# Optimization experiments

Measured on AMD Instinct MI355X. Metric: run time of the kernel, lower is better.

## Reference

```python
import jax, jax.numpy as jnp
import numpy as np

H = 2048; FF = 8192; NH = 16; HD = 128; R = 16; SCALING = 2.0  # alpha/r = 32/16
EPS = 1e-5
NLEV = 15.0  # 2**4 - 1 levels for 4-bit quantization

def _quantize(key, out_f, in_f):
    # mirrors QuantizedLinear.quantize_weights on a randn*0.02 init weight
    w = jax.random.normal(key, (out_f, in_f), dtype=jnp.float32) * 0.02
    wmin = w.min(axis=1, keepdims=True)
    wmax = w.max(axis=1, keepdims=True)
    rng = jnp.clip(wmax - wmin, 1e-6)
    sc = rng / NLEV
    q = jnp.clip(jnp.round((w - wmin) / sc), 0, NLEV).astype(jnp.int8)
    return q, sc[:, 0], wmin[:, 0]

def setup_inputs():
    key = jax.random.key(0)
    ks = jax.random.split(key, 22)
    dims = [('q', H, H), ('k', H, H), ('v', H, H), ('o', H, H), ('g', FF, H), ('u', FF, H), ('d', H, FF)]
    d = {}
    i = 0
    for name, of, inf in dims:
        qw, sc, zp = _quantize(ks[i], of, inf); i += 1
        d[name + '_qw'] = qw; d[name + '_sc'] = sc; d[name + '_zp'] = zp
        d[name + '_A'] = jax.random.normal(ks[i], (R, inf), dtype=jnp.float32) * 0.01; i += 1
        d[name + '_B'] = jax.random.normal(ks[i], (of, R), dtype=jnp.float32) * 0.01; i += 1
    d['x'] = jax.random.normal(ks[i], (2, 2048, H), dtype=jnp.float32)
    d['ln1_w'] = jnp.ones(H); d['ln1_b'] = jnp.zeros(H)
    d['ln2_w'] = jnp.ones(H); d['ln2_b'] = jnp.zeros(H)
    return d

def _forward(x, qws, ps, lns):
    def lin(h, i):
        sc, zp, A, B = ps[i]
        # dequantize int8 weight (per-row scale/zero-point) + LoRA low-rank update
        W = qws[i].astype(jnp.float32) * sc[:, None] + zp[:, None] + (B @ A) * SCALING
        return h @ W.T
    def ln(h, w, b):
        mu = h.mean(-1, keepdims=True)
        var = h.var(-1, keepdims=True)  # biased, matches torch LayerNorm
        return (h - mu) / jnp.sqrt(var + EPS) * w + b
    ln1_w, ln1_b, ln2_w, ln2_b = lns
    Bsz, S, _ = x.shape
    h = ln(x, ln1_w, ln1_b)
    q = lin(h, 0).reshape(Bsz, S, NH, HD)
    k = lin(h, 1).reshape(Bsz, S, NH, HD)
    v = lin(h, 2).reshape(Bsz, S, NH, HD)
    attn = jnp.einsum('bqhd,bkhd->bhqk', q, k) / (HD ** 0.5)
    attn = jax.nn.softmax(attn, axis=-1)  # dropout is identity in eval
    o = jnp.einsum('bhqk,bkhd->bqhd', attn, v).reshape(Bsz, S, H)
    x1 = x + lin(o, 3)
    h2 = ln(x1, ln2_w, ln2_b)
    ff = jax.nn.silu(lin(h2, 4)) * lin(h2, 5)
    return x1 + lin(ff, 6)

def reference(x, q_qw, q_sc, q_zp, q_A, q_B, k_qw, k_sc, k_zp, k_A, k_B, v_qw, v_sc, v_zp, v_A, v_B, o_qw, o_sc, o_zp, o_A, o_B, g_qw, g_sc, g_zp, g_A, g_B, u_qw, u_sc, u_zp, u_A, u_B, d_qw, d_sc, d_zp, d_A, d_B, ln1_w, ln1_b, ln2_w, ln2_b):
    qws = (q_qw, k_qw, v_qw, o_qw, g_qw, u_qw, d_qw)
    ps = [(q_sc, q_zp, q_A, q_B), (k_sc, k_zp, k_A, k_B), (v_sc, v_zp, v_A, v_B), (o_sc, o_zp, o_A, o_B), (g_sc, g_zp, g_A, g_B), (u_sc, u_zp, u_A, u_B), (d_sc, d_zp, d_A, d_B)]
    return _forward(x, qws, ps, (ln1_w, ln1_b, ln2_w, ln2_b))
```

## Files before the change

### kernel.cpp

```cpp
#include <hip/hip_runtime.h>
#include <cstdint>
#include <cstddef>

#define GLOBAL_AS __attribute__((address_space(1)))
#define LDS_AS    __attribute__((address_space(3)))

typedef __bf16 bf16;
typedef __bf16 bf16x4 __attribute__((ext_vector_type(4)));
typedef __bf16 bf16x8 __attribute__((ext_vector_type(8)));
typedef float  f32x4  __attribute__((ext_vector_type(4)));
typedef int    i32x4  __attribute__((ext_vector_type(4)));
typedef unsigned int u32x2 __attribute__((ext_vector_type(2)));

__device__ __forceinline__ void gl_lds16(const void* g, void* l) {
  __builtin_amdgcn_global_load_lds((GLOBAL_AS void*)g, (LDS_AS void*)l, 16, 0, 0);
}

__global__ __launch_bounds__(256) void ln_kernel(const float* __restrict__ x,
                                                 const float* __restrict__ w,
                                                 const float* __restrict__ bias,
                                                 bf16* __restrict__ out) {
  const int row = blockIdx.x;
  const int tid = threadIdx.x;
  const float* xr = x + (size_t)row * 2048;
  f32x4 v0 = ((const f32x4*)xr)[tid * 2];
  f32x4 v1 = ((const f32x4*)xr)[tid * 2 + 1];
  float s = 0.f, ss = 0.f;
#pragma unroll
  for (int j = 0; j < 4; ++j) { s += v0[j]; ss += v0[j] * v0[j]; }
#pragma unroll
  for (int j = 0; j < 4; ++j) { s += v1[j]; ss += v1[j] * v1[j]; }
#pragma unroll
  for (int d = 1; d < 64; d <<= 1) { s += __shfl_xor(s, d); ss += __shfl_xor(ss, d); }
  __shared__ float red[8];
  const int wave = tid >> 6, lane = tid & 63;
  if (lane == 0) { red[wave * 2] = s; red[wave * 2 + 1] = ss; }
  __syncthreads();
  s  = red[0] + red[2] + red[4] + red[6];
  ss = red[1] + red[3] + red[5] + red[7];
  const float mean = s * (1.f / 2048.f);
  const float var  = ss * (1.f / 2048.f) - mean * mean;
  const float rstd = rsqrtf(var + 1e-5f);
  const int col = tid * 8;
  bf16x8 o;
#pragma unroll
  for (int j = 0; j < 4; ++j) o[j]     = (bf16)((v0[j] - mean) * rstd * w[col + j]     + bias[col + j]);
#pragma unroll
  for (int j = 0; j < 4; ++j) o[4 + j] = (bf16)((v1[j] - mean) * rstd * w[col + 4 + j] + bias[col + 4 + j]);
  *(bf16x8*)(out + (size_t)row * 2048 + col) = o;
}

__global__ __launch_bounds__(256) void ln_q_kernel(const float* __restrict__ x,
    const float* __restrict__ w, const float* __restrict__ bias,
    char* __restrict__ qh, float* __restrict__ s_m, float* __restrict__ rs,
    float* __restrict__ de) {
  const int row = blockIdx.x;
  const int tid = threadIdx.x;
  const float* xr = x + (size_t)row * 2048;
  f32x4 v0 = ((const f32x4*)xr)[tid * 2];
  f32x4 v1 = ((const f32x4*)xr)[tid * 2 + 1];
  float s = 0.f, ss = 0.f;
#pragma unroll
  for (int j = 0; j < 4; ++j) { s += v0[j]; ss += v0[j] * v0[j]; }
#pragma unroll
  for (int j = 0; j < 4; ++j) { s += v1[j]; ss += v1[j] * v1[j]; }
#pragma unroll
  for (int d = 1; d < 64; d <<= 1) { s += __shfl_xor(s, d); ss += __shfl_xor(ss, d); }
  __shared__ float red[12];
  const int wave = tid >> 6, lane = tid & 63;
  if (lane == 0) { red[wave * 2] = s; red[wave * 2 + 1] = ss; }
  __syncthreads();
  s  = red[0] + red[2] + red[4] + red[6];
  ss = red[1] + red[3] + red[5] + red[7];
  const float mean = s * (1.f / 2048.f);
  const float var  = ss * (1.f / 2048.f) - mean * mean;
  const float rstd = rsqrtf(var + 1e-5f);
  const int col = tid * 8;
  float y[8];
#pragma unroll
  for (int j = 0; j < 4; ++j) y[j]     = (v0[j] - mean) * rstd * w[col + j]     + bias[col + j];
#pragma unroll
  for (int j = 0; j < 4; ++j) y[4 + j] = (v1[j] - mean) * rstd * w[col + 4 + j] + bias[col + 4 + j];
  float sy = 0.f, mx = 0.f;
#pragma unroll
  for (int j = 0; j < 8; ++j) { sy += y[j]; mx = fmaxf(mx, fabsf(y[j])); }
#pragma unroll
  for (int d = 1; d < 64; d <<= 1) { sy += __shfl_xor(sy, d); mx = fmaxf(mx, __shfl_xor(mx, d)); }
  __syncthreads();
  if (lane == 0) { red[wave * 2] = sy; red[wave * 2 + 1] = mx; }
  __syncthreads();
  const float sya = red[0] + red[2] + red[4] + red[6];
  const float mxa = fmaxf(fmaxf(red[1], red[3]), fmaxf(red[5], red[7]));
  const float inv = 127.f / fmaxf(mxa, 1e-8f);
  unsigned int lo = 0, hi = 0;
  int qs = 0;
#pragma unroll
  for (int j = 0; j < 4; ++j) { int qi = (int)rintf(y[j] * inv);     qs += qi; lo |= ((unsigned int)qi & 0xffu) << (8 * j); }
#pragma unroll
  for (int j = 0; j < 4; ++j) { int qi = (int)rintf(y[4 + j] * inv); qs += qi; hi |= ((unsigned int)qi & 0xffu) << (8 * j); }
  u32x2 st; st[0] = lo; st[1] = hi;
  *(u32x2*)(qh + (size_t)row * 2048 + col) = st;
  float fqs = (float)qs;
#pragma unroll
  for (int d = 1; d < 64; d <<= 1) fqs += __shfl_xor(fqs, d);
  __syncthreads();
  if (lane == 0) red[8 + wave] = fqs;
  __syncthreads();
  if (tid == 0) {
    const float qsa = red[8] + red[9] + red[10] + red[11];
    const float smv = fmaxf(mxa, 1e-8f) / 127.f;
    s_m[row] = smv; rs[row] = sya; de[row] = sya - smv * qsa;
  }
}

__global__ __launch_bounds__(256) void dequant_kernel(const int* __restrict__ qw,
    const float* __restrict__ sc, const float* __restrict__ zp,
    const float* __restrict__ A, const float* __restrict__ Bm,
    bf16* __restrict__ W, int out_f, int in_f) {
  const int per_row = in_f >> 3;
  const int idx = blockIdx.x * 256 + threadIdx.x;
  const int o  = idx / per_row;
  const int i0 = (idx - o * per_row) << 3;
  const float s = sc[o], z = zp[o];
  float bl[16];
#pragma unroll
  for (int r = 0; r < 16; ++r) bl[r] = Bm[o * 16 + r];
  float acc[8] = {0.f, 0.f, 0.f, 0.f, 0.f, 0.f, 0.f, 0.f};
#pragma unroll
  for (int r = 0; r < 16; ++r) {
    const f32x4* ap = (const f32x4*)(A + (size_t)r * in_f + i0);
    f32x4 a0 = ap[0], a1 = ap[1];
#pragma unroll
    for (int j = 0; j < 4; ++j) { acc[j] += bl[r] * a0[j]; acc[4 + j] += bl[r] * a1[j]; }
  }
  const int* qp = qw + (size_t)o * in_f + i0;
  bf16x8 w8;
#pragma unroll
  for (int j = 0; j < 8; ++j) w8[j] = (bf16)((float)qp[j] * s + z + 2.f * acc[j]);
  *(bf16x8*)(W + (size_t)o * in_f + i0) = w8;
}

__global__ __launch_bounds__(256) void pack_w_kernel(const int* __restrict__ qw,
    const float* __restrict__ sc, char* __restrict__ out, float* __restrict__ wsum) {
  const int row = blockIdx.x;
  const int tid = threadIdx.x;
  const size_t idx = (size_t)row * 2048 + tid * 8;
  i32x4 a = *(const i32x4*)(qw + idx);
  i32x4 b = *(const i32x4*)(qw + idx + 4);
  unsigned int lo = ((unsigned)a[0] & 0xffu) | (((unsigned)a[1] & 0xffu) << 8) |
                    (((unsigned)a[2] & 0xffu) << 16) | (((unsigned)a[3] & 0xffu) << 24);
  unsigned int hi = ((unsigned)b[0] & 0xffu) | (((unsigned)b[1] & 0xffu) << 8) |
                    (((unsigned)b[2] & 0xffu) << 16) | (((unsigned)b[3] & 0xffu) << 24);
  u32x2 st; st[0] = lo; st[1] = hi;
  *(u32x2*)(out + idx) = st;
  float fs = (float)(a[0] + a[1] + a[2] + a[3] + b[0] + b[1] + b[2] + b[3]);
#pragma unroll
  for (int d = 1; d < 64; d <<= 1) fs += __shfl_xor(fs, d);
  __shared__ float red[4];
  const int wave = tid >> 6, lane = tid & 63;
  if (lane == 0) red[wave] = fs;
  __syncthreads();
  if (tid == 0) wsum[row] = sc[row] * (red[0] + red[1] + red[2] + red[3]) * (1.f / 2048.f);
}

__global__ __launch_bounds__(256) void pack_b2_kernel(const float* __restrict__ gB,
    const float* __restrict__ uB, bf16* __restrict__ B2g, bf16* __restrict__ B2u) {
  const int idx = blockIdx.x * 256 + threadIdx.x;
  const int nn = idx >> 5, r = idx & 31;
  B2g[idx] = (r < 16)  ? (bf16)(2.f * gB[nn * 16 + r])        : (bf16)0.f;
  B2u[idx] = (r >= 16) ? (bf16)(2.f * uB[nn * 16 + (r - 16)]) : (bf16)0.f;
}

__global__ __launch_bounds__(256) void hA_kernel(const char* __restrict__ qh,
    const float* __restrict__ s_m, const float* __restrict__ Ag,
    const float* __restrict__ Au, bf16* __restrict__ hA) {
  __shared__ bf16 Asm[32 * 512];
  const int tid = threadIdx.x, wave = tid >> 6, lane = tid & 63;
  const int row = blockIdx.x * 4 + wave;
  float acc[32];
#pragma unroll
  for (int r = 0; r < 32; ++r) acc[r] = 0.f;
  for (int kb = 0; kb < 2048; kb += 512) {
    const int r2 = tid >> 3, c0 = (tid & 7) * 64;
    const float* src = (r2 < 16 ? Ag + (size_t)r2 * 2048 : Au + (size_t)(r2 - 16) * 2048) + kb + c0;
#pragma unroll
    for (int j = 0; j < 64; j += 8) {
      f32x4 va = *(const f32x4*)(src + j);
      f32x4 vb = *(const f32x4*)(src + j + 4);
      bf16x8 bv;
#pragma unroll
      for (int jj = 0; jj < 4; ++jj) { bv[jj] = (bf16)va[jj]; bv[4 + jj] = (bf16)vb[jj]; }
      *(bf16x8*)(Asm + r2 * 512 + c0 + j) = bv;
    }
    __syncthreads();
    float q[8];
    const char* qp = qh + (size_t)row * 2048 + kb + lane * 8;
#pragma unroll
    for (int j = 0; j < 8; ++j) q[j] = (float)qp[j];
#pragma unroll
    for (int r = 0; r < 32; ++r) {
      bf16x8 a8 = *(const bf16x8*)(Asm + r * 512 + lane * 8);
      float d = 0.f;
#pragma unroll
      for (int j = 0; j < 8; ++j) d += q[j] * (float)a8[j];
      acc[r] += d;
    }
    __syncthreads();
  }
  const float s = s_m[row];
#pragma unroll
  for (int r = 0; r < 32; ++r) {
    float v = acc[r];
#pragma unroll
    for (int d = 1; d < 64; d <<= 1) v += __shfl_xor(v, d);
    if (lane == 0) hA[(size_t)row * 32 + r] = (bf16)(s * v);
  }
}

#define STAGE_A(t, buf, r8) gl_lds16(Ag + (size_t)(r8) * 8 * K + (size_t)(t) * 64, \
                                     &As[buf][((wave * 32) + (r8) * 8) * 64])
#define STAGE_B(t, buf, r8) gl_lds16(Bg + (size_t)(r8) * 8 * K + (size_t)(t) * 64, \
                                     &Bs[buf][((wave * 16) + (r8) * 8) * 64])

template <int MODE>
__global__ __launch_bounds__(512, 2) void gemm8_kernel(const bf16* __restrict__ A,
    const bf16* __restrict__ B, bf16* __restrict__ Cb, float* __restrict__ Cf,
    const float* __restrict__ res, bf16* __restrict__ vt,
    int M, int N, int K, int ldc) {
  const int tid = threadIdx.x;
  const int wave = tid >> 6, lane = tid & 63;
  const int lcol = lane & 15, lrow = lane >> 4;
  const int wm = (wave >> 1) * 64, wn = (wave & 1) * 64;
  const int nwg = gridDim.x * gridDim.y;
  const int bid = blockIdx.y * gridDim.x + blockIdx.x;
  const int swb = (bid & 7) * (nwg >> 3) + (bid >> 3);
  const int n0 = (swb % gridDim.x) * 128;
  const int m0 = (swb / gridDim.x) * 256;
  __shared__ bf16 As[3][256 * 64];
  __shared__ bf16 Bs[3][128 * 64];
  f32x4 acc[4][4] = {};
  const int sw = ((lane & 7) ^ ((lane >> 3) & 7)) * 8;
  const bf16* Ag = A + (size_t)(m0 + wave * 32 + (lane >> 3)) * K + sw;
  const bf16* Bg = B + (size_t)(n0 + wave * 16 + (lane >> 3)) * K + sw;
  const int nt = K >> 6;

#pragma unroll
  for (int r8 = 0; r8 < 4; ++r8) STAGE_A(0, 0, r8);
  STAGE_B(0, 0, 0); STAGE_B(0, 0, 1);
#pragma unroll
  for (int r8 = 0; r8 < 4; ++r8) STAGE_A(1, 1, r8);
  STAGE_B(1, 1, 0); STAGE_B(1, 1, 1);
  asm volatile("s_waitcnt vmcnt(6)" ::: "memory");
  __builtin_amdgcn_s_barrier();

  int cur = 0;
  for (int t = 0; t < nt; ++t) {
    const bf16* Ac = As[cur];
    const bf16* Bc = Bs[cur];
    const int nx = (cur >= 1) ? cur - 1 : 2;
    const bool pf = (t + 2 < nt);

    bf16x8 a0[4], b0[4];
#pragma unroll
    for (int j = 0; j < 4; ++j)
      b0[j] = *(const bf16x8*)(Bc + (wn + j * 16 + lcol) * 64 + (lrow ^ (lcol & 7)) * 8);
#pragma unroll
    for (int i = 0; i < 4; ++i)
      a0[i] = *(const bf16x8*)(Ac + (wm + i * 16 + lcol) * 64 + (lrow ^ (lcol & 7)) * 8);
    if (pf) { STAGE_A(t + 2, nx, 0); STAGE_A(t + 2, nx, 1); STAGE_B(t + 2, nx, 0); }
    __builtin_amdgcn_s_barrier();
    __builtin_amdgcn_s_setprio(1);
#pragma unroll
    for (int i = 0; i < 4; ++i)
#pragma unroll
      for (int j = 0; j < 4; ++j)
        acc[i][j] = __builtin_amdgcn_mfma_f32_16x16x32_bf16(a0[i], b0[j], acc[i][j], 0, 0, 0);
    __builtin_amdgcn_s_setprio(0);
    __builtin_amdgcn_s_barrier();

    bf16x8 a1[4], b1[4];
#pragma unroll
    for (int j = 0; j < 4; ++j)
      b1[j] = *(const bf16x8*)(Bc + (wn + j * 16 + lcol) * 64 + ((4 + lrow) ^ (lcol & 7)) * 8);
#pragma unroll
    for (int i = 0; i < 4; ++i)
      a1[i] = *(const bf16x8*)(Ac + (wm + i * 16 + lcol) * 64 + ((4 + lrow) ^ (lcol & 7)) * 8);
    if (pf) { STAGE_A(t + 2, nx, 2); STAGE_A(t + 2, nx, 3); STAGE_B(t + 2, nx, 1); }
    __builtin_amdgcn_s_barrier();
    __builtin_amdgcn_s_setprio(1);
#pragma unroll
    for (int i = 0; i < 4; ++i)
#pragma unroll
      for (int j = 0; j < 4; ++j)
        acc[i][j] = __builtin_amdgcn_mfma_f32_16x16x32_bf16(a1[i], b1[j], acc[i][j], 0, 0, 0);
    __builtin_amdgcn_s_setprio(0);
    if (pf) asm volatile("s_waitcnt vmcnt(6)" ::: "memory");
    else    asm volatile("s_waitcnt vmcnt(0)" ::: "memory");
    __builtin_amdgcn_s_barrier();
    cur = (cur == 2) ? 0 : cur + 1;
  }

#pragma unroll
  for (int i = 0; i < 4; ++i)
#pragma unroll
    for (int j = 0; j < 4; ++j) {
      const int row0 = m0 + wm + i * 16 + lrow * 4;
      const int col  = n0 + wn + j * 16 + lcol;
      if (MODE == 3 && col >= 4096) {
        const int c2 = col - 4096;
        bf16x4 v4;
#pragma unroll
        for (int r = 0; r < 4; ++r) v4[r] = (bf16)acc[i][j][r];
        *(bf16x4*)(vt + (size_t)(((row0 >> 11) * 16 + (c2 >> 7)) * 128 + (c2 & 127)) * 2048
                      + (row0 & 2047)) = v4;
      } else {
#pragma unroll
        for (int r = 0; r < 4; ++r) {
          const int row = row0 + r;
          const float v = acc[i][j][r];
          const size_t idx = (size_t)row * ldc + col;
          if (MODE == 1) Cf[idx] = res[idx] + v;
          else           Cb[idx] = (bf16)v;
        }
      }
    }
}
#undef STAGE_A
#undef STAGE_B

template <int MODE>
__global__ __launch_bounds__(256) void gemm_i8_kernel(const char* __restrict__ Aq,
    const char* __restrict__ Bq, const float* __restrict__ s_m, const float* __restrict__ rs,
    const float* __restrict__ de, const float* __restrict__ sc, const float* __restrict__ zp,
    const float* __restrict__ wsum, const bf16* __restrict__ hA, const bf16* __restrict__ B2,
    bf16* __restrict__ Cb, const bf16* __restrict__ gate, int M, int N, int K) {
  const int nwg = gridDim.x * gridDim.y;
  const int bid = blockIdx.y * gridDim.x + blockIdx.x;
  const int swb = (bid & 7) * (nwg >> 3) + (bid >> 3);
  const int n0 = (swb % gridDim.x) * 128;
  const int m0 = (swb / gridDim.x) * 128;
  const int tid = threadIdx.x;
  const int wave = tid >> 6, lane = tid & 63;
  const int lcol = lane & 15, lrow = lane >> 4;
  const int wm = (wave >> 1) * 64, wn = (wave & 1) * 64;
  __shared__ char As[128 * 128];
  __shared__ char Bs[128 * 128];
  i32x4 acc[4][4] = {};
  const int sw = (((lane & 7) ^ ((lane >> 3) & 7))) * 16;
  const char* Ag = Aq + (size_t)(m0 + wave * 32 + (lane >> 3)) * K + sw;
  const char* Bg = Bq + (size_t)(n0 + wave * 32 + (lane >> 3)) * K + sw;
  for (int kt = 0; kt < K; kt += 128) {
#pragma unroll
    for (int r8 = 0; r8 < 4; ++r8) {
      gl_lds16(Ag + (size_t)r8 * 8 * K + kt, As + (wave * 32 + r8 * 8) * 128);
      gl_lds16(Bg + (size_t)r8 * 8 * K + kt, Bs + (wave * 32 + r8 * 8) * 128);
    }
    __syncthreads();
#pragma unroll
    for (int ks = 0; ks < 2; ++ks) {
      i32x4 af[4], bfr[4];
#pragma unroll
      for (int i = 0; i < 4; ++i)
        af[i]  = *(const i32x4*)(As + (wm + i * 16 + lcol) * 128 + (((ks * 4 + lrow) ^ (lcol & 7))) * 16);
#pragma unroll
      for (int j = 0; j < 4; ++j)
        bfr[j] = *(const i32x4*)(Bs + (wn + j * 16 + lcol) * 128 + (((ks * 4 + lrow) ^ (lcol & 7))) * 16);
#pragma unroll
      for (int i = 0; i < 4; ++i)
#pragma unroll
        for (int j = 0; j < 4; ++j)
          acc[i][j] = __builtin_amdgcn_mfma_i32_16x16x64_i8(af[i], bfr[j], acc[i][j], 0, 0, 0);
    }
    __syncthreads();
  }
  bf16x8 ha[4], bb[4];
#pragma unroll
  for (int i = 0; i < 4; ++i) ha[i] = *(const bf16x8*)(hA + (size_t)(m0 + wm + i * 16 + lcol) * 32 + lrow * 8);
#pragma unroll
  for (int j = 0; j < 4; ++j) bb[j] = *(const bf16x8*)(B2 + (size_t)(n0 + wn + j * 16 + lcol) * 32 + lrow * 8);
  float scv[4], zpv[4], wsv[4];
#pragma unroll
  for (int j = 0; j < 4; ++j) {
    const int col = n0 + wn + j * 16 + lcol;
    scv[j] = sc[col]; zpv[j] = zp[col]; wsv[j] = wsum[col];
  }
  float smv[4][4], rsv[4][4], dev[4][4];
#pragma unroll
  for (int i = 0; i < 4; ++i)
#pragma unroll
    for (int r = 0; r < 4; ++r) {
      const int row = m0 + wm + i * 16 + lrow * 4 + r;
      smv[i][r] = s_m[row]; rsv[i][r] = rs[row]; dev[i][r] = de[row];
    }
  const f32x4 zero = {0.f, 0.f, 0.f, 0.f};
#pragma unroll
  for (int i = 0; i < 4; ++i)
#pragma unroll
    for (int j = 0; j < 4; ++j) {
      f32x4 L = __builtin_amdgcn_mfma_f32_16x16x32_bf16(ha[i], bb[j], zero, 0, 0, 0);
#pragma unroll
      for (int r = 0; r < 4; ++r) {
        const int row = m0 + wm + i * 16 + lrow * 4 + r;
        const int col = n0 + wn + j * 16 + lcol;
        const float v = scv[j] * smv[i][r] * (float)acc[i][j][r] + zpv[j] * rsv[i][r]
                      + wsv[j] * dev[i][r] + L[r];
        const size_t idx = (size_t)row * N + col;
        if (MODE == 0) Cb[idx] = (bf16)v;
        else {
          const float g = (float)gate[idx];
          Cb[idx] = (bf16)((g / (1.f + __expf(-g))) * v);
        }
      }
    }
}

__global__ __launch_bounds__(256) void attn_kernel(const bf16* __restrict__ Cqk,
                                                   const bf16* __restrict__ VtG,
                                                   bf16* __restrict__ obuf) {
  const int qt = blockIdx.x, h = blockIdx.y, b = blockIdx.z;
  const int tid = threadIdx.x, wave = tid >> 6, lane = tid & 63;
  const int lcol = lane & 15, lrow = lane >> 4;
  const int base_m = b * 2048 + qt * 128;
  __shared__ bf16 Ks[64 * 128];
  __shared__ bf16 Vt[128 * 64];
  __shared__ bf16 Ps[4][32 * 72];
  bf16* ps = Ps[wave];
  bf16x8 qf[2][4];
#pragma unroll
  for (int i = 0; i < 2; ++i)
#pragma unroll
    for (int dk = 0; dk < 4; ++dk)
      qf[i][dk] = *(const bf16x8*)(Cqk + (size_t)(base_m + wave * 32 + i * 16 + lcol) * 4096
                                   + h * 128 + dk * 32 + lrow * 8);
  f32x4 of[2][8] = {};
  float m_run[2][4], l_run[2][4];
#pragma unroll
  for (int i = 0; i < 2; ++i)
#pragma unroll
    for (int r = 0; r < 4; ++r) { m_run[i][r] = -1e30f; l_run[i][r] = 0.f; }
  const float SCL2 = 0.12751874972f;
  const int vswz = (lane & 7) ^ (lane >> 3);

  for (int kt = 0; kt < 2048; kt += 64) {
#pragma unroll
    for (int r4 = 0; r4 < 4; ++r4) {
      const int s_low = r4 * 4 + lrow;
      gl_lds16(Cqk + (size_t)(b * 2048 + kt + wave * 16 + s_low) * 4096 + 2048 + h * 128
                   + (lcol ^ s_low) * 8,
               Ks + (wave * 16 + r4 * 4) * 128);
    }
#pragma unroll
    for (int r8 = 0; r8 < 4; ++r8)
      gl_lds16(VtG + (size_t)((b * 16 + h) * 128 + wave * 32 + r8 * 8 + (lane >> 3)) * 2048
                   + kt + vswz * 8,
               Vt + (wave * 32 + r8 * 8) * 64);
    __syncthreads();

    f32x4 sacc[2][4] = {};
#pragma unroll
    for (int jb = 0; jb < 4; ++jb) {
      bf16x8 kf[4];
#pragma unroll
      for (int dk = 0; dk < 4; ++dk)
        kf[dk] = *(const bf16x8*)(Ks + (jb * 16 + lcol) * 128 + ((dk * 4 + lrow) ^ lcol) * 8);
#pragma unroll
      for (int i = 0; i < 2; ++i)
#pragma unroll
        for (int dk = 0; dk < 4; ++dk)
          sacc[i][jb] = __builtin_amdgcn_mfma_f32_16x16x32_bf16(qf[i][dk], kf[dk], sacc[i][jb], 0, 0, 0);
    }

#pragma unroll
    for (int i = 0; i < 2; ++i) {
      float z[4][4], mx[4];
#pragma unroll
      for (int jb = 0; jb < 4; ++jb)
#pragma unroll
        for (int r = 0; r < 4; ++r) z[jb][r] = sacc[i][jb][r] * SCL2;
#pragma unroll
      for (int r = 0; r < 4; ++r)
        mx[r] = fmaxf(fmaxf(z[0][r], z[1][r]), fmaxf(z[2][r], z[3][r]));
#pragma unroll
      for (int d = 1; d < 16; d <<= 1)
#pragma unroll
        for (int r = 0; r < 4; ++r) mx[r] = fmaxf(mx[r], __shfl_xor(mx[r], d));
#pragma unroll
      for (int r = 0; r < 4; ++r) {
        const float mn = fmaxf(m_run[i][r], mx[r]);
        const float alpha = __builtin_amdgcn_exp2f(m_run[i][r] - mn);
        m_run[i][r] = mn;
        float srow = 0.f;
#pragma unroll
        for (int jb = 0; jb < 4; ++jb) {
          const float p = __builtin_amdgcn_exp2f(z[jb][r] - mn);
          z[jb][r] = p; srow += p;
        }
        l_run[i][r] = l_run[i][r] * alpha + srow;
#pragma unroll
        for (int db = 0; db < 8; ++db) of[i][db][r] *= alpha;
      }
#pragma unroll
      for (int jb = 0; jb < 4; ++jb)
#pragma unroll
        for (int r = 0; r < 4; ++r)
          ps[(i * 16 + lrow * 4 + r) * 72 + jb * 16 + lcol] = (bf16)z[jb][r];
    }

#pragma unroll
    for (int ss = 0; ss < 2; ++ss) {
      bf16x8 a0 = *(const bf16x8*)(ps + (0 * 16 + lcol) * 72 + ss * 32 + lrow * 8);
      bf16x8 a1 = *(const bf16x8*)(ps + (1 * 16 + lcol) * 72 + ss * 32 + lrow * 8);
#pragma unroll
      for (int db = 0; db < 8; ++db) {
        bf16x8 vf = *(const bf16x8*)(Vt + (db * 16 + lcol) * 64 + ((ss * 4 + lrow) ^ (lcol & 7)) * 8);
        of[0][db] = __builtin_amdgcn_mfma_f32_16x16x32_bf16(a0, vf, of[0][db], 0, 0, 0);
        of[1][db] = __builtin_amdgcn_mfma_f32_16x16x32_bf16(a1, vf, of[1][db], 0, 0, 0);
      }
    }
    __syncthreads();
  }
#pragma unroll
  for (int i = 0; i < 2; ++i)
#pragma unroll
    for (int r = 0; r < 4; ++r) {
      float l = l_run[i][r];
#pragma unroll
      for (int d = 1; d < 16; d <<= 1) l += __shfl_xor(l, d);
      const float inv = 1.f / l;
      const size_t rb = (size_t)(base_m + wave * 32 + i * 16 + lrow * 4 + r) * 2048 + h * 128;
#pragma unroll
      for (int db = 0; db < 8; ++db)
        obuf[rb + db * 16 + lcol] = (bf16)(of[i][db][r] * inv);
    }
}

extern "C" void kernel_launch(void* const* d_in, const int* in_sizes, int n_in,
                              void* d_out, int out_size, void* d_ws, size_t ws_size,
                              hipStream_t stream) {
  (void)in_sizes; (void)n_in; (void)out_size; (void)ws_size;
  const int*   q_qw = (const int*)d_in[0];   const float* q_sc = (const float*)d_in[1];
  const float* q_zp = (const float*)d_in[2]; const float* q_A  = (const float*)d_in[3];
  const float* q_B  = (const float*)d_in[4];
  const int*   k_qw = (const int*)d_in[5];   const float* k_sc = (const float*)d_in[6];
  const float* k_zp = (const float*)d_in[7]; const float* k_A  = (const float*)d_in[8];
  const float* k_B  = (const float*)d_in[9];
  const int*   v_qw = (const int*)d_in[10];  const float* v_sc = (const float*)d_in[11];
  const float* v_zp = (const float*)d_in[12];const float* v_A  = (const float*)d_in[13];
  const float* v_B  = (const float*)d_in[14];
  const int*   o_qw = (const int*)d_in[15];  const float* o_sc = (const float*)d_in[16];
  const float* o_zp = (const float*)d_in[17];const float* o_A  = (const float*)d_in[18];
  const float* o_B  = (const float*)d_in[19];
  const int*   g_qw = (const int*)d_in[20];  const float* g_sc = (const float*)d_in[21];
  const float* g_zp = (const float*)d_in[22];const float* g_A  = (const float*)d_in[23];
  const float* g_B  = (const float*)d_in[24];
  const int*   u_qw = (const int*)d_in[25];  const float* u_sc = (const float*)d_in[26];
  const float* u_zp = (const float*)d_in[27];const float* u_A  = (const float*)d_in[28];
  const float* u_B  = (const float*)d_in[29];
  const int*   d_qw = (const int*)d_in[30];  const float* d_sc = (const float*)d_in[31];
  const float* d_zp = (const float*)d_in[32];const float* d_A  = (const float*)d_in[33];
  const float* d_B  = (const float*)d_in[34];
  const float* x    = (const float*)d_in[35];
  const float* ln1w = (const float*)d_in[36];const float* ln1b = (const float*)d_in[37];
  const float* ln2w = (const float*)d_in[38];const float* ln2b = (const float*)d_in[39];

  char* ws = (char*)d_ws;
  bf16* W = (bf16*)ws;
  char* Wg8 = ws;
  char* Wu8 = ws + (size_t)8192 * 2048;
  char* p2  = ws + (size_t)32 * 1024 * 1024;
  bf16* h   = (bf16*)p2;
  char*  qh  = p2;
  float* s_m = (float*)(p2 + 8 * 1024 * 1024);
  float* rs  = (float*)(p2 + 8 * 1024 * 1024 + 16384);
  float* de  = (float*)(p2 + 8 * 1024 * 1024 + 32768);
  bf16*  hA  = (bf16*)(p2 + 8 * 1024 * 1024 + 49152);
  bf16*  B2g = (bf16*)(p2 + 8 * 1024 * 1024 + 49152 + 262144);
  bf16*  B2u = B2g + (size_t)8192 * 32;
  float* wsg = (float*)((char*)(B2u + (size_t)8192 * 32));
  float* wsu = wsg + 8192;
  bf16* C = (bf16*)(ws + (size_t)48 * 1024 * 1024);
  bf16* Cqk = C;
  bf16* VtG = C + (size_t)4096 * 4096;
  bf16* obuf = VtG + (size_t)2 * 16 * 128 * 2048;
  float* x1  = (float*)d_out;
  float* out = (float*)d_out;

  ln_kernel<<<4096, 256, 0, stream>>>(x, ln1w, ln1b, h);
  dequant_kernel<<<2048, 256, 0, stream>>>(q_qw, q_sc, q_zp, q_A, q_B, W, 2048, 2048);
  dequant_kernel<<<2048, 256, 0, stream>>>(k_qw, k_sc, k_zp, k_A, k_B, W + (size_t)2048 * 2048, 2048, 2048);
  dequant_kernel<<<2048, 256, 0, stream>>>(v_qw, v_sc, v_zp, v_A, v_B, W + (size_t)4096 * 2048, 2048, 2048);
  gemm8_kernel<3><<<dim3(48, 16), 512, 0, stream>>>(h, W, Cqk, nullptr, nullptr, VtG, 4096, 6144, 2048, 4096);
  attn_kernel<<<dim3(16, 16, 2), 256, 0, stream>>>(Cqk, VtG, obuf);
  dequant_kernel<<<2048, 256, 0, stream>>>(o_qw, o_sc, o_zp, o_A, o_B, W, 2048, 2048);
  gemm8_kernel<1><<<dim3(16, 16), 512, 0, stream>>>(obuf, W, nullptr, x1, x, nullptr, 4096, 2048, 2048, 2048);
  ln_q_kernel<<<4096, 256, 0, stream>>>(x1, ln2w, ln2b, qh, s_m, rs, de);
  hA_kernel<<<1024, 256, 0, stream>>>(qh, s_m, g_A, u_A, hA);
  pack_w_kernel<<<8192, 256, 0, stream>>>(g_qw, g_sc, Wg8, wsg);
  pack_w_kernel<<<8192, 256, 0, stream>>>(u_qw, u_sc, Wu8, wsu);
  pack_b2_kernel<<<1024, 256, 0, stream>>>(g_B, u_B, B2g, B2u);
  gemm_i8_kernel<0><<<dim3(64, 32), 256, 0, stream>>>(qh, Wg8, s_m, rs, de, g_sc, g_zp, wsg, hA, B2g, C, nullptr, 4096, 8192, 2048);
  gemm_i8_kernel<1><<<dim3(64, 32), 256, 0, stream>>>(qh, Wu8, s_m, rs, de, u_sc, u_zp, wsu, hA, B2u, C, C, 4096, 8192, 2048);
  dequant_kernel<<<8192, 256, 0, stream>>>(d_qw, d_sc, d_zp, d_A, d_B, W, 2048, 8192);
  gemm8_kernel<1><<<dim3(16, 16), 512, 0, stream>>>(C, W, nullptr, out, x1, nullptr, 4096, 2048, 8192, 2048);
}
```

Before: 1.172 ms.

## Triple-buffer the int8 GEMM with a 256x128 tile and 8-wave blocks

```diff
diff --git a/kernel.cpp b/kernel.cpp
--- a/kernel.cpp
+++ b/kernel.cpp
@@ -328,51 +328,90 @@
 #undef STAGE_A
 #undef STAGE_B
 
+#define STAGE_A8(t, buf, r8) gl_lds16(Ag + (size_t)(r8) * 8 * K + (size_t)(t) * 128, \
+                                      &As[buf][((wave * 32) + (r8) * 8) * 128])
+#define STAGE_B8(t, buf, r8) gl_lds16(Bg + (size_t)(r8) * 8 * K + (size_t)(t) * 128, \
+                                      &Bs[buf][((wave * 16) + (r8) * 8) * 128])
+
 template <int MODE>
-__global__ __launch_bounds__(256) void gemm_i8_kernel(const char* __restrict__ Aq,
+__global__ __launch_bounds__(512, 2) void gemm_i8_kernel(const char* __restrict__ Aq,
     const char* __restrict__ Bq, const float* __restrict__ s_m, const float* __restrict__ rs,
     const float* __restrict__ de, const float* __restrict__ sc, const float* __restrict__ zp,
     const float* __restrict__ wsum, const bf16* __restrict__ hA, const bf16* __restrict__ B2,
     bf16* __restrict__ Cb, const bf16* __restrict__ gate, int M, int N, int K) {
+  const int tid = threadIdx.x;
+  const int wave = tid >> 6, lane = tid & 63;
+  const int lcol = lane & 15, lrow = lane >> 4;
+  const int wm = (wave >> 1) * 64, wn = (wave & 1) * 64;
   const int nwg = gridDim.x * gridDim.y;
   const int bid = blockIdx.y * gridDim.x + blockIdx.x;
   const int swb = (bid & 7) * (nwg >> 3) + (bid >> 3);
   const int n0 = (swb % gridDim.x) * 128;
-  const int m0 = (swb / gridDim.x) * 128;
-  const int tid = threadIdx.x;
-  const int wave = tid >> 6, lane = tid & 63;
-  const int lcol = lane & 15, lrow = lane >> 4;
-  const int wm = (wave >> 1) * 64, wn = (wave & 1) * 64;
-  __shared__ char As[128 * 128];
-  __shared__ char Bs[128 * 128];
+  const int m0 = (swb / gridDim.x) * 256;
+  __shared__ char As[3][256 * 128];
+  __shared__ char Bs[3][128 * 128];
   i32x4 acc[4][4] = {};
-  const int sw = (((lane & 7) ^ ((lane >> 3) & 7))) * 16;
+  const int sw = ((lane & 7) ^ ((lane >> 3) & 7)) * 16;
   const char* Ag = Aq + (size_t)(m0 + wave * 32 + (lane >> 3)) * K + sw;
-  const char* Bg = Bq + (size_t)(n0 + wave * 32 + (lane >> 3)) * K + sw;
-  for (int kt = 0; kt < K; kt += 128) {
-#pragma unroll
-    for (int r8 = 0; r8 < 4; ++r8) {
-      gl_lds16(Ag + (size_t)r8 * 8 * K + kt, As + (wave * 32 + r8 * 8) * 128);
-      gl_lds16(Bg + (size_t)r8 * 8 * K + kt, Bs + (wave * 32 + r8 * 8) * 128);
-    }
-    __syncthreads();
-#pragma unroll
-    for (int ks = 0; ks < 2; ++ks) {
-      i32x4 af[4], bfr[4];
-#pragma unroll
-      for (int i = 0; i < 4; ++i)
-        af[i]  = *(const i32x4*)(As + (wm + i * 16 + lcol) * 128 + (((ks * 4 + lrow) ^ (lcol & 7))) * 16);
+  const char* Bg = Bq + (size_t)(n0 + wave * 16 + (lane >> 3)) * K + sw;
+  const int nt = K >> 7;
+
+#pragma unroll
+  for (int r8 = 0; r8 < 4; ++r8) STAGE_A8(0, 0, r8);
+  STAGE_B8(0, 0, 0); STAGE_B8(0, 0, 1);
+#pragma unroll
+  for (int r8 = 0; r8 < 4; ++r8) STAGE_A8(1, 1, r8);
+  STAGE_B8(1, 1, 0); STAGE_B8(1, 1, 1);
+  asm volatile("s_waitcnt vmcnt(6)" ::: "memory");
+  __builtin_amdgcn_s_barrier();
+
+  int cur = 0;
+  for (int t = 0; t < nt; ++t) {
+    const char* Ac = As[cur];
+    const char* Bc = Bs[cur];
+    const int nx = (cur >= 1) ? cur - 1 : 2;
+    const bool pf = (t + 2 < nt);
+
+    i32x4 af0[4], bf0[4];
+#pragma unroll
+    for (int j = 0; j < 4; ++j)
+      bf0[j] = *(const i32x4*)(Bc + (wn + j * 16 + lcol) * 128 + (lrow ^ (lcol & 7)) * 16);
+#pragma unroll
+    for (int i = 0; i < 4; ++i)
+      af0[i] = *(const i32x4*)(Ac + (wm + i * 16 + lcol) * 128 + (lrow ^ (lcol & 7)) * 16);
+    if (pf) { STAGE_A8(t + 2, nx, 0); STAGE_A8(t + 2, nx, 1); STAGE_B8(t + 2, nx, 0); }
+    __builtin_amdgcn_s_barrier();
+    __builtin_amdgcn_s_setprio(1);
+#pragma unroll
+    for (int i = 0; i < 4; ++i)
 #pragma unroll
       for (int j = 0; j < 4; ++j)
-        bfr[j] = *(const i32x4*)(Bs + (wn + j * 16 + lcol) * 128 + (((ks * 4 + lrow) ^ (lcol & 7))) * 16);
-#pragma unroll
-      for (int i = 0; i < 4; ++i)
-#pragma unroll
-        for (int j = 0; j < 4; ++j)
-          acc[i][j] = __builtin_amdgcn_mfma_i32_16x16x64_i8(af[i], bfr[j], acc[i][j], 0, 0, 0);
-    }
-    __syncthreads();
-  }
+        acc[i][j] = __builtin_amdgcn_mfma_i32_16x16x64_i8(af0[i], bf0[j], acc[i][j], 0, 0, 0);
+    __builtin_amdgcn_s_setprio(0);
+    __builtin_amdgcn_s_barrier();
+
+    i32x4 af1[4], bf1[4];
+#pragma unroll
+    for (int j = 0; j < 4; ++j)
+      bf1[j] = *(const i32x4*)(Bc + (wn + j * 16 + lcol) * 128 + ((4 + lrow) ^ (lcol & 7)) * 16);
+#pragma unroll
+    for (int i = 0; i < 4; ++i)
+      af1[i] = *(const i32x4*)(Ac + (wm + i * 16 + lcol) * 128 + ((4 + lrow) ^ (lcol & 7)) * 16);
+    if (pf) { STAGE_A8(t + 2, nx, 2); STAGE_A8(t + 2, nx, 3); STAGE_B8(t + 2, nx, 1); }
+    __builtin_amdgcn_s_barrier();
+    __builtin_amdgcn_s_setprio(1);
+#pragma unroll
+    for (int i = 0; i < 4; ++i)
+#pragma unroll
+      for (int j = 0; j < 4; ++j)
+        acc[i][j] = __builtin_amdgcn_mfma_i32_16x16x64_i8(af1[i], bf1[j], acc[i][j], 0, 0, 0);
+    __builtin_amdgcn_s_setprio(0);
+    if (pf) asm volatile("s_waitcnt vmcnt(6)" ::: "memory");
+    else    asm volatile("s_waitcnt vmcnt(0)" ::: "memory");
+    __builtin_amdgcn_s_barrier();
+    cur = (cur == 2) ? 0 : cur + 1;
+  }
+
   bf16x8 ha[4], bb[4];
 #pragma unroll
   for (int i = 0; i < 4; ++i) ha[i] = *(const bf16x8*)(hA + (size_t)(m0 + wm + i * 16 + lcol) * 32 + lrow * 8);
@@ -413,6 +452,8 @@
       }
     }
 }
+#undef STAGE_A8
+#undef STAGE_B8
 
 __global__ __launch_bounds__(256) void attn_kernel(const bf16* __restrict__ Cqk,
                                                    const bf16* __restrict__ VtG,
@@ -598,8 +639,8 @@
   pack_w_kernel<<<8192, 256, 0, stream>>>(g_qw, g_sc, Wg8, wsg);
   pack_w_kernel<<<8192, 256, 0, stream>>>(u_qw, u_sc, Wu8, wsu);
   pack_b2_kernel<<<1024, 256, 0, stream>>>(g_B, u_B, B2g, B2u);
-  gemm_i8_kernel<0><<<dim3(64, 32), 256, 0, stream>>>(qh, Wg8, s_m, rs, de, g_sc, g_zp, wsg, hA, B2g, C, nullptr, 4096, 8192, 2048);
-  gemm_i8_kernel<1><<<dim3(64, 32), 256, 0, stream>>>(qh, Wu8, s_m, rs, de, u_sc, u_zp, wsu, hA, B2u, C, C, 4096, 8192, 2048);
+  gemm_i8_kernel<0><<<dim3(64, 16), 512, 0, stream>>>(qh, Wg8, s_m, rs, de, g_sc, g_zp, wsg, hA, B2g, C, nullptr, 4096, 8192, 2048);
+  gemm_i8_kernel<1><<<dim3(64, 16), 512, 0, stream>>>(qh, Wu8, s_m, rs, de, u_sc, u_zp, wsu, hA, B2u, C, C, 4096, 8192, 2048);
   dequant_kernel<<<8192, 256, 0, stream>>>(d_qw, d_sc, d_zp, d_A, d_B, W, 2048, 8192);
   gemm8_kernel<1><<<dim3(16, 16), 512, 0, stream>>>(C, W, nullptr, out, x1, nullptr, 4096, 2048, 8192, 2048);
 }
```

Measured after the change: 1.127 ms. 3.8% less time.
